# Kernel tuning notes

Measured on AMD Instinct MI355X. Metric: run time of the kernel, lower is better.

The kernel has to match this reference:

```python
import jax, jax.numpy as jnp
import numpy as np

# Sizes: N news nodes, E 'similar' edges, 768-d input, hidden 64, 4 heads, 2 HGT layers, 2 classes
N, E, F_IN, HID, H, L, C = 100000, 1600000, 768, 64, 4, 2, 2
D = HID // H  # per-head dim = 16


def setup_inputs() -> dict:
    key = jax.random.key(0)
    ks = jax.random.split(key, 16)
    s = 0.05
    nrm = lambda k, shape: jax.random.normal(k, shape, jnp.float32) * s
    return {
        "x": jax.random.normal(ks[0], (N, F_IN), jnp.float32),
        "edge_index": jax.random.randint(ks[1], (2, E), 0, N, jnp.int32),
        # input projection
        "Wp": nrm(ks[2], (F_IN, HID)), "bp": jnp.zeros((HID,), jnp.float32),
        # per-layer HGT params (stacked over L layers)
        "Wk": nrm(ks[3], (L, HID, HID)), "bk": jnp.zeros((L, HID), jnp.float32),
        "Wq": nrm(ks[4], (L, HID, HID)), "bq": jnp.zeros((L, HID), jnp.float32),
        "Wv": nrm(ks[5], (L, HID, HID)), "bv": jnp.zeros((L, HID), jnp.float32),
        "a_rel": nrm(ks[6], (L, H, D, D)),  # per-edge-type attention transform
        "m_rel": nrm(ks[7], (L, H, D, D)),  # per-edge-type message transform
        "p_rel": jnp.ones((L, H), jnp.float32),  # relation prior
        "Wo": nrm(ks[8], (L, HID, HID)), "bo": jnp.zeros((L, HID), jnp.float32),
        "skip": jnp.ones((L,), jnp.float32),
        # classifier MLP: 64 -> 32 -> 2
        "Wc1": nrm(ks[9], (HID, HID // 2)), "bc1": jnp.zeros((HID // 2,), jnp.float32),
        "Wc2": nrm(ks[10], (HID // 2, C)), "bc2": jnp.zeros((C,), jnp.float32),
    }


def _hgt_layer(h, src, dst, Wk, bk, Wq, bq, Wv, bv, a_rel, m_rel, p_rel, Wo, bo, skip):
    n = h.shape[0]
    k = (h @ Wk + bk).reshape(n, H, D)
    q = (h @ Wq + bq).reshape(n, H, D)
    v = (h @ Wv + bv).reshape(n, H, D)
    # per-edge attention logits: (k_src @ a_rel) . q_dst * p_rel / sqrt(D)
    k_e = jnp.einsum('ehd,hdf->ehf', k[src], a_rel)          # [E,H,D]
    alpha = jnp.einsum('ehf,ehf->eh', k_e, q[dst]) * p_rel / np.float32(np.sqrt(D))
    # segment softmax over incoming edges of each dst node
    mx = jax.ops.segment_max(alpha, dst, num_segments=n)     # [N,H]
    a = jnp.exp(alpha - mx[dst])
    denom = jax.ops.segment_sum(a, dst, num_segments=n)
    a = a / (denom[dst] + 1e-16)
    # messages + scatter-add aggregation
    msg = jnp.einsum('ehd,hdf->ehf', v[src], m_rel)          # [E,H,D]
    agg = jax.ops.segment_sum(a[..., None] * msg, dst, num_segments=n).reshape(n, HID)
    out = jax.nn.gelu(agg) @ Wo + bo
    g = jax.nn.sigmoid(skip)
    return g * out + (1.0 - g) * h  # skip connection (same dims)


def reference(x, edge_index, Wp, bp, Wk, bk, Wq, bq, Wv, bv, a_rel, m_rel, p_rel,
              Wo, bo, skip, Wc1, bc1, Wc2, bc2):
    src, dst = edge_index[0], edge_index[1]
    h = x @ Wp + bp
    for l in range(L):
        h = _hgt_layer(h, src, dst, Wk[l], bk[l], Wq[l], bq[l], Wv[l], bv[l],
                       a_rel[l], m_rel[l], p_rel[l], Wo[l], bo[l], skip[l])
        h = jax.nn.relu(h)  # dropout is identity in eval mode
    hc = jax.nn.relu(h @ Wc1 + bc1)
    return hc @ Wc2 + bc2  # [N, C] logits
```

## Files before the change

kernel.cpp:

```cpp
#include <hip/hip_runtime.h>
#include <math.h>


typedef __attribute__((ext_vector_type(8))) short bf16x8;
typedef __attribute__((ext_vector_type(4))) float f32x4;

__device__ __forceinline__ float gelu_t(float x) {
  const float c = 0.7978845608028654f;
  float t = tanhf(c * (x + 0.044715f * x * x * x));
  return 0.5f * x * (1.0f + t);
}

__device__ __forceinline__ void split1(float a, ushort& h, ushort& l) {
  unsigned u = __float_as_uint(a);
  unsigned uh = u & 0xffff0000u;
  float fl = a - __uint_as_float(uh);
  h = (ushort)(uh >> 16);
  l = (ushort)(__float_as_uint(fl) >> 16);
}

template<int K, bool PRE_GELU, bool EPI_SKIP>
__global__ __launch_bounds__(256, 4)
void mfma_gemm(const float* __restrict__ A, int ldA,
               const ushort* __restrict__ Wt,
               const float* __restrict__ bias,
               const float* __restrict__ Hprev,
               const float* __restrict__ skipPtr,
               float* __restrict__ outp, int ldOut, int nRows)
{
  constexpr int NCH = K / 32;
  __shared__ ushort sA[2 * 64 * 32];
  __shared__ ushort sB[2 * 64 * 32];
  const int tid = threadIdx.x;
  const int lane = tid & 63;
  const int wv = tid >> 6;
  const int m = lane & 15;
  const int q = lane >> 4;
  const int row0 = blockIdx.x * 64;
  const int colBlk = blockIdx.y * 64;

  const int srow = tid >> 2;
  const int skoff = (tid & 3) * 8;
  int gr = row0 + srow; if (gr >= nRows) gr = nRows - 1;
  const float* aBase = A + (size_t)gr * ldA + skoff;
  const float4* wBase = (const float4*)(Wt + (size_t)blockIdx.y * NCH * 4096);

  f32x4 acc[4];
#pragma unroll
  for (int ct = 0; ct < 4; ++ct) acc[ct] = (f32x4){0.f, 0.f, 0.f, 0.f};

  float4 a0 = *(const float4*)(aBase + 0);
  float4 a1 = *(const float4*)(aBase + 4);
  float4 b0 = wBase[tid * 2];
  float4 b1 = wBase[tid * 2 + 1];

#pragma clang loop unroll(disable)
  for (int ch = 0; ch < NCH; ++ch) {
    float4 na0 = a0, na1 = a1, nb0 = b0, nb1 = b1;
    if (ch + 1 < NCH) {
      na0 = *(const float4*)(aBase + (ch + 1) * 32);
      na1 = *(const float4*)(aBase + (ch + 1) * 32 + 4);
      const float4* wc = wBase + (size_t)(ch + 1) * 512;
      nb0 = wc[tid * 2];
      nb1 = wc[tid * 2 + 1];
    }
    float av[8] = {a0.x, a0.y, a0.z, a0.w, a1.x, a1.y, a1.z, a1.w};
    if (PRE_GELU) {
#pragma unroll
      for (int j = 0; j < 8; ++j) av[j] = gelu_t(av[j]);
    }
    bf16x8 vh, vl;
#pragma unroll
    for (int j = 0; j < 8; ++j) {
      ushort h, l; split1(av[j], h, l);
      vh[j] = (short)h; vl[j] = (short)l;
    }
    __syncthreads();
    *(bf16x8*)(sA + srow * 32 + skoff) = vh;
    *(bf16x8*)(sA + 2048 + srow * 32 + skoff) = vl;
    ((float4*)sB)[tid * 2] = b0;
    ((float4*)sB)[tid * 2 + 1] = b1;
    __syncthreads();
    bf16x8 ah = *(const bf16x8*)(sA + (wv * 16 + m) * 32 + q * 8);
    bf16x8 al = *(const bf16x8*)(sA + 2048 + (wv * 16 + m) * 32 + q * 8);
#pragma unroll
    for (int ct = 0; ct < 4; ++ct) {
      bf16x8 bh = *(const bf16x8*)(sB + (ct * 16 + m) * 32 + q * 8);
      bf16x8 bl = *(const bf16x8*)(sB + 2048 + (ct * 16 + m) * 32 + q * 8);
      acc[ct] = __builtin_amdgcn_mfma_f32_16x16x32_bf16(ah, bh, acc[ct], 0, 0, 0);
      acc[ct] = __builtin_amdgcn_mfma_f32_16x16x32_bf16(ah, bl, acc[ct], 0, 0, 0);
      acc[ct] = __builtin_amdgcn_mfma_f32_16x16x32_bf16(al, bh, acc[ct], 0, 0, 0);
    }
    a0 = na0; a1 = na1; b0 = nb0; b1 = nb1;
  }

  float g = 0.f, gi = 0.f;
  if (EPI_SKIP) { g = 1.0f / (1.0f + __expf(-skipPtr[0])); gi = 1.0f - g; }
#pragma unroll
  for (int ct = 0; ct < 4; ++ct) {
    int c = colBlk + ct * 16 + m;
    float b = bias[c];
#pragma unroll
    for (int i = 0; i < 4; ++i) {
      int r = row0 + wv * 16 + q * 4 + i;
      if (r < nRows) {
        float o = acc[ct][i] + b;
        if (EPI_SKIP) {
          float hp = Hprev[(size_t)r * 64 + c];
          o = fmaxf(g * o + gi * hp, 0.f);
        }
        outp[(size_t)r * ldOut + c] = o;
      }
    }
  }
}

__global__ void prep_weights(const float* __restrict__ W, int K, int C,
                             ushort* __restrict__ Wt)
{
  int idx = blockIdx.x * 256 + threadIdx.x;
  if (idx < K * C) {
    int k = idx / C, c = idx % C;
    ushort h, l; split1(W[idx], h, l);
    int cb = c >> 6, cc = c & 63, ch = k >> 5, kk = k & 31;
    size_t base = (size_t)(cb * (K >> 5) + ch) * 4096;
    Wt[base + cc * 32 + kk] = h;
    Wt[base + 2048 + cc * 32 + kk] = l;
  }
}

__global__ void fold_weights(const float* __restrict__ Wq, const float* __restrict__ bq,
                             const float* __restrict__ Wk, const float* __restrict__ bk,
                             const float* __restrict__ Wv, const float* __restrict__ bv,
                             const float* __restrict__ a_rel, const float* __restrict__ m_rel,
                             float* __restrict__ Wqkv, float* __restrict__ bqkv)
{
  int l = blockIdx.x;
  const float* wq = Wq + l * 4096; const float* wk = Wk + l * 4096; const float* wv = Wv + l * 4096;
  const float* bql = bq + l * 64;  const float* bkl = bk + l * 64;  const float* bvl = bv + l * 64;
  const float* ar = a_rel + l * 1024; const float* mr = m_rel + l * 1024;
  float* W = Wqkv + l * 64 * 192;  float* B = bqkv + l * 192;
  for (int t = threadIdx.x; t < 64 * 192; t += blockDim.x) {
    int i = t / 192, c = t % 192;
    float val;
    int cp;
    if (c < 64) {
      val = wq[i * 64 + c];
      cp = c;
    } else if (c < 128) {
      int cc = c - 64, hh = cc >> 4, f = cc & 15;
      float s = 0.f;
      for (int d = 0; d < 16; ++d) s += wk[i * 64 + hh * 16 + d] * ar[hh * 256 + d * 16 + f];
      val = s;
      cp = 64 + (cc << 1);
    } else {
      int cc = c - 128, hh = cc >> 4, f = cc & 15;
      float s = 0.f;
      for (int d = 0; d < 16; ++d) s += wv[i * 64 + hh * 16 + d] * mr[hh * 256 + d * 16 + f];
      val = s;
      cp = 64 + (cc << 1) + 1;
    }
    W[i * 192 + cp] = val;
  }
  for (int c = threadIdx.x; c < 192; c += blockDim.x) {
    float val;
    int cp;
    if (c < 64) {
      val = bql[c];
      cp = c;
    } else if (c < 128) {
      int cc = c - 64, hh = cc >> 4, f = cc & 15;
      float s = 0.f;
      for (int d = 0; d < 16; ++d) s += bkl[hh * 16 + d] * ar[hh * 256 + d * 16 + f];
      val = s;
      cp = 64 + (cc << 1);
    } else {
      int cc = c - 128, hh = cc >> 4, f = cc & 15;
      float s = 0.f;
      for (int d = 0; d < 16; ++d) s += bvl[hh * 16 + d] * mr[hh * 256 + d * 16 + f];
      val = s;
      cp = 64 + (cc << 1) + 1;
    }
    B[cp] = val;
  }
}

__global__ void hist_kernel(const int* __restrict__ dst, int* __restrict__ counts, int E) {
  int e = blockIdx.x * 256 + threadIdx.x;
  if (e < E) atomicAdd(&counts[dst[e]], 1);
}

__global__ __launch_bounds__(256)
void scanA(int* __restrict__ counts, int* __restrict__ blockSums, int n) {
  __shared__ int sd[256];
  int tid = threadIdx.x;
  int base = blockIdx.x * 1024 + tid * 4;
  int v[4];
#pragma unroll
  for (int j = 0; j < 4; ++j) v[j] = (base + j < n) ? counts[base + j] : 0;
  int t = v[0] + v[1] + v[2] + v[3];
  sd[tid] = t; __syncthreads();
  for (int offm = 1; offm < 256; offm <<= 1) {
    int adj = (tid >= offm) ? sd[tid - offm] : 0;
    __syncthreads();
    sd[tid] += adj;
    __syncthreads();
  }
  int run = sd[tid] - t;
#pragma unroll
  for (int j = 0; j < 4; ++j) {
    if (base + j < n) counts[base + j] = run;
    run += v[j];
  }
  if (tid == 255) blockSums[blockIdx.x] = sd[255];
}

__global__ void scanB(int* __restrict__ blockSums, int G, int* __restrict__ row_ptr, int n) {
  __shared__ int sd[128];
  int tid = threadIdx.x;
  int t = (tid < G) ? blockSums[tid] : 0;
  sd[tid] = t; __syncthreads();
  for (int offm = 1; offm < 128; offm <<= 1) {
    int adj = (tid >= offm) ? sd[tid - offm] : 0;
    __syncthreads();
    sd[tid] += adj;
    __syncthreads();
  }
  if (tid < G) blockSums[tid] = sd[tid] - t;
  if (tid == 127) row_ptr[n] = sd[127];
}

__global__ void scanC(const int* __restrict__ counts, const int* __restrict__ blockSums,
                      int* __restrict__ row_ptr, int* __restrict__ cursor, int n) {
  int idx = blockIdx.x * 256 + threadIdx.x;
  if (idx < n) {
    int v = counts[idx] + blockSums[idx >> 10];
    row_ptr[idx] = v;
    cursor[idx] = v;
  }
}

__global__ void scatter_kernel(const int* __restrict__ src, const int* __restrict__ dst,
                               int* __restrict__ cursor, int* __restrict__ csr_src, int E) {
  int e = blockIdx.x * 256 + threadIdx.x;
  if (e < E) {
    int d = dst[e];
    int pos = atomicAdd(&cursor[d], 1);
    csr_src[pos] = src[e];
  }
}

__global__ __launch_bounds__(256)
void edge_agg(const float* __restrict__ qkv, const int* __restrict__ row_ptr,
              const int* __restrict__ csr_src, const float* __restrict__ p_rel,
              float* __restrict__ agg, int n)
{
  int wid = blockIdx.x * 4 + (threadIdx.x >> 6);
  if (wid >= n) return;
  int lane = threadIdx.x & 63;
  int head = lane >> 4;
  float pr = p_rel[head] * 0.25f;
  float qv = qkv[(size_t)wid * 192 + lane] * pr;
  int e0 = row_ptr[wid], e1 = row_ptr[wid + 1];
  float num = 0.f, den = 0.f;
  for (int e = e0; e < e1; e += 4) {
    int last = e1 - 1;
    int ia = e;
    int ib = (e + 1 < e1) ? e + 1 : last;
    int ic = (e + 2 < e1) ? e + 2 : last;
    int id = (e + 3 < e1) ? e + 3 : last;
    int s0 = csr_src[ia];
    int s1 = csr_src[ib];
    int s2 = csr_src[ic];
    int s3 = csr_src[id];
    float2 kv0 = *(const float2*)(qkv + (size_t)s0 * 192 + 64 + 2 * lane);
    float2 kv1 = *(const float2*)(qkv + (size_t)s1 * 192 + 64 + 2 * lane);
    float2 kv2 = *(const float2*)(qkv + (size_t)s2 * 192 + 64 + 2 * lane);
    float2 kv3 = *(const float2*)(qkv + (size_t)s3 * 192 + 64 + 2 * lane);
    float p0 = kv0.x * qv;
    float p1 = kv1.x * qv;
    float p2 = kv2.x * qv;
    float p3 = kv3.x * qv;
#pragma unroll
    for (int o = 1; o < 16; o <<= 1) {
      p0 += __shfl_xor(p0, o);
      p1 += __shfl_xor(p1, o);
      p2 += __shfl_xor(p2, o);
      p3 += __shfl_xor(p3, o);
    }
    float w0 = __expf(p0);
    float w1 = (e + 1 < e1) ? __expf(p1) : 0.f;
    float w2 = (e + 2 < e1) ? __expf(p2) : 0.f;
    float w3 = (e + 3 < e1) ? __expf(p3) : 0.f;
    den += (w0 + w1) + (w2 + w3);
    num = fmaf(w0, kv0.y, num);
    num = fmaf(w1, kv1.y, num);
    num = fmaf(w2, kv2.y, num);
    num = fmaf(w3, kv3.y, num);
  }
  agg[(size_t)wid * 64 + lane] = num / (den + 1e-16f);
}

__global__ __launch_bounds__(256)
void classifier(const float* __restrict__ h, const float* __restrict__ Wc1,
                const float* __restrict__ bc1, const float* __restrict__ Wc2,
                const float* __restrict__ bc2, float* __restrict__ out, int n)
{
  int row = blockIdx.x * 256 + threadIdx.x;
  if (row >= n) return;
  float hid[32];
#pragma unroll
  for (int j = 0; j < 32; ++j) hid[j] = bc1[j];
  const float* hr = h + (size_t)row * 64;
#pragma unroll 4
  for (int k = 0; k < 64; k += 4) {
    float4 x = *(const float4*)&hr[k];
#pragma unroll
    for (int j = 0; j < 32; ++j) {
      hid[j] += x.x * Wc1[k * 32 + j] + x.y * Wc1[(k + 1) * 32 + j]
              + x.z * Wc1[(k + 2) * 32 + j] + x.w * Wc1[(k + 3) * 32 + j];
    }
  }
  float o0 = bc2[0], o1 = bc2[1];
#pragma unroll
  for (int j = 0; j < 32; ++j) {
    float v = fmaxf(hid[j], 0.f);
    o0 += v * Wc2[j * 2 + 0];
    o1 += v * Wc2[j * 2 + 1];
  }
  *(float2*)&out[(size_t)row * 2] = make_float2(o0, o1);
}

extern "C" void kernel_launch(void* const* d_in, const int* in_sizes, int n_in,
                              void* d_out, int out_size, void* d_ws, size_t ws_size,
                              hipStream_t stream)
{
  const float* x     = (const float*)d_in[0];
  const int*  eidx   = (const int*)d_in[1];
  const float* Wp    = (const float*)d_in[2];
  const float* bp    = (const float*)d_in[3];
  const float* Wk    = (const float*)d_in[4];
  const float* bk    = (const float*)d_in[5];
  const float* Wq    = (const float*)d_in[6];
  const float* bq    = (const float*)d_in[7];
  const float* Wv    = (const float*)d_in[8];
  const float* bv    = (const float*)d_in[9];
  const float* a_rel = (const float*)d_in[10];
  const float* m_rel = (const float*)d_in[11];
  const float* p_rel = (const float*)d_in[12];
  const float* Wo    = (const float*)d_in[13];
  const float* bo    = (const float*)d_in[14];
  const float* skip  = (const float*)d_in[15];
  const float* Wc1   = (const float*)d_in[16];
  const float* bc1   = (const float*)d_in[17];
  const float* Wc2   = (const float*)d_in[18];
  const float* bc2   = (const float*)d_in[19];
  float* out = (float*)d_out;

  const int N = in_sizes[0] / 768;
  const int E = in_sizes[1] / 2;
  const int* srcIdx = eidx;
  const int* dstIdx = eidx + E;

  char* ws = (char*)d_ws;
  size_t off = 0;
  auto alloc = [&](size_t bytes) -> void* {
    void* p = ws + off;
    off = (off + bytes + 255) & ~(size_t)255;
    return p;
  };
  float* h     = (float*)alloc((size_t)N * 64 * 4);
  float* qkv   = (float*)alloc((size_t)N * 192 * 4);
  float* agg   = (float*)alloc((size_t)N * 64 * 4);
  float* Wqkv  = (float*)alloc(2 * 64 * 192 * 4);
  float* bqkv  = (float*)alloc(2 * 192 * 4);
  int* row_ptr = (int*)alloc((size_t)(N + 1) * 4);
  int* cursor  = (int*)alloc((size_t)N * 4);
  int* counts  = (int*)alloc((size_t)N * 4);
  int* blockSums = (int*)alloc(512 * 4);
  int* csr_src = (int*)alloc((size_t)E * 4);
  ushort* WtP   = (ushort*)alloc((size_t)64 * 768 * 2 * 2);
  ushort* WtQKV = (ushort*)alloc((size_t)2 * 192 * 64 * 2 * 2);
  ushort* WtO   = (ushort*)alloc((size_t)2 * 64 * 64 * 2 * 2);
  (void)ws_size; (void)n_in; (void)out_size;

  hipMemsetAsync(counts, 0, (size_t)N * 4, stream);

  fold_weights<<<2, 256, 0, stream>>>(Wq, bq, Wk, bk, Wv, bv, a_rel, m_rel, Wqkv, bqkv);

  prep_weights<<<(768 * 64 + 255) / 256, 256, 0, stream>>>(Wp, 768, 64, WtP);
  for (int l = 0; l < 2; ++l) {
    prep_weights<<<(64 * 192 + 255) / 256, 256, 0, stream>>>(
        Wqkv + l * 64 * 192, 64, 192, WtQKV + (size_t)l * 192 * 64 * 2);
    prep_weights<<<(64 * 64 + 255) / 256, 256, 0, stream>>>(
        Wo + l * 4096, 64, 64, WtO + (size_t)l * 64 * 64 * 2);
  }

  mfma_gemm<768, false, false><<<dim3((N + 63) / 64, 1), 256, 0, stream>>>(
      x, 768, WtP, bp, nullptr, nullptr, h, 64, N);

  hist_kernel<<<(E + 255) / 256, 256, 0, stream>>>(dstIdx, counts, E);
  int G = (N + 1023) / 1024;
  scanA<<<G, 256, 0, stream>>>(counts, blockSums, N);
  scanB<<<1, 128, 0, stream>>>(blockSums, G, row_ptr, N);
  scanC<<<(N + 255) / 256, 256, 0, stream>>>(counts, blockSums, row_ptr, cursor, N);
  scatter_kernel<<<(E + 255) / 256, 256, 0, stream>>>(srcIdx, dstIdx, cursor, csr_src, E);

  for (int l = 0; l < 2; ++l) {
    mfma_gemm<64, false, false><<<dim3((N + 63) / 64, 3), 256, 0, stream>>>(
        h, 64, WtQKV + (size_t)l * 192 * 64 * 2, bqkv + l * 192,
        nullptr, nullptr, qkv, 192, N);
    edge_agg<<<(N + 3) / 4, 256, 0, stream>>>(qkv, row_ptr, csr_src, p_rel + l * 4, agg, N);
    mfma_gemm<64, true, true><<<dim3((N + 63) / 64, 1), 256, 0, stream>>>(
        agg, 64, WtO + (size_t)l * 64 * 64 * 2, bo + l * 64, h, skip + l, h, 64, N);
  }

  classifier<<<(N + 255) / 256, 256, 0, stream>>>(h, Wc1, bc1, Wc2, bc2, out, N);
}
```

Baseline: 1.054 ms.

## Add specialized K=64 MFMA GEMM and unroll edge aggregation with DPP reductions

Adds a K=64-specialized split-bf16 MFMA GEMM. It loads the whole A tile once and computes all 192 QKV columns in one block instead of three grid columns, which avoids re-reading and re-splitting A per column block. The edge aggregation kernel now processes 8 edges per iteration and uses readfirstlane to make the neighbor indices scalar. Its 16-lane dot-product reduction uses DPP row_ror instead of shuffles. This raises register and LDS use (launch bounds drop to 2) in exchange for fewer redundant loads and more memory-level parallelism.

After: 1.071 ms. About the same (+1.6%).

```diff
diff --git a/kernel.cpp b/kernel.cpp
--- a/kernel.cpp
+++ b/kernel.cpp
@@ -17,6 +17,19 @@
   float fl = a - __uint_as_float(uh);
   h = (ushort)(uh >> 16);
   l = (ushort)(__float_as_uint(fl) >> 16);
+}
+
+template<int CTRL>
+__device__ __forceinline__ float row_ror_add(float v) {
+  int r = __builtin_amdgcn_update_dpp(0, __float_as_int(v), CTRL, 0xF, 0xF, true);
+  return v + __int_as_float(r);
+}
+__device__ __forceinline__ float red16(float v) {
+  v = row_ror_add<0x121>(v);
+  v = row_ror_add<0x122>(v);
+  v = row_ror_add<0x124>(v);
+  v = row_ror_add<0x128>(v);
+  return v;
 }
 
 template<int K, bool PRE_GELU, bool EPI_SKIP>
@@ -110,6 +123,125 @@
           o = fmaxf(g * o + gi * hp, 0.f);
         }
         outp[(size_t)r * ldOut + c] = o;
+      }
+    }
+  }
+}
+
+template<int CB, bool PRE_GELU, bool EPI_SKIP>
+__global__ __launch_bounds__(256, 2)
+void mfma_gemm_k64(const float* __restrict__ A,
+                   const ushort* __restrict__ Wt,
+                   const float* __restrict__ bias,
+                   const float* __restrict__ Hprev,
+                   const float* __restrict__ skipPtr,
+                   float* __restrict__ outp, int ldOut, int nRows)
+{
+  __shared__ ushort sA[2 * 4096];
+  __shared__ ushort sB[CB][2 * 4096];
+  const int tid = threadIdx.x;
+  const int lane = tid & 63;
+  const int wv = tid >> 6;
+  const int m = lane & 15;
+  const int q = lane >> 4;
+  const int row0 = blockIdx.x * 64;
+  const int srow = tid >> 2;
+  const int skoff = (tid & 3) * 8;
+  int gr = row0 + srow; if (gr >= nRows) gr = nRows - 1;
+  const float* aBase = A + (size_t)gr * 64 + skoff;
+  const float4* wBase = (const float4*)Wt;
+
+  float4 a0 = *(const float4*)(aBase + 0);
+  float4 a1 = *(const float4*)(aBase + 4);
+  float4 a2 = *(const float4*)(aBase + 32);
+  float4 a3 = *(const float4*)(aBase + 36);
+  float4 bb0[CB], bb1[CB], bb2[CB], bb3[CB];
+#pragma unroll
+  for (int cb = 0; cb < CB; ++cb) {
+    bb0[cb] = wBase[(size_t)(cb * 2 + 0) * 512 + tid * 2];
+    bb1[cb] = wBase[(size_t)(cb * 2 + 0) * 512 + tid * 2 + 1];
+    bb2[cb] = wBase[(size_t)(cb * 2 + 1) * 512 + tid * 2];
+    bb3[cb] = wBase[(size_t)(cb * 2 + 1) * 512 + tid * 2 + 1];
+  }
+
+  {
+    float av[16] = {a0.x, a0.y, a0.z, a0.w, a1.x, a1.y, a1.z, a1.w,
+                    a2.x, a2.y, a2.z, a2.w, a3.x, a3.y, a3.z, a3.w};
+    if (PRE_GELU) {
+#pragma unroll
+      for (int j = 0; j < 16; ++j) av[j] = gelu_t(av[j]);
+    }
+    bf16x8 vh0, vl0, vh1, vl1;
+#pragma unroll
+    for (int j = 0; j < 8; ++j) {
+      ushort h, l; split1(av[j], h, l);
+      vh0[j] = (short)h; vl0[j] = (short)l;
+    }
+#pragma unroll
+    for (int j = 0; j < 8; ++j) {
+      ushort h, l; split1(av[8 + j], h, l);
+      vh1[j] = (short)h; vl1[j] = (short)l;
+    }
+    *(bf16x8*)(sA + srow * 32 + skoff) = vh0;
+    *(bf16x8*)(sA + 2048 + srow * 32 + skoff) = vl0;
+    *(bf16x8*)(sA + 4096 + srow * 32 + skoff) = vh1;
+    *(bf16x8*)(sA + 4096 + 2048 + srow * 32 + skoff) = vl1;
+  }
+#pragma unroll
+  for (int cb = 0; cb < CB; ++cb) {
+    ((float4*)(sB[cb]))[tid * 2] = bb0[cb];
+    ((float4*)(sB[cb]))[tid * 2 + 1] = bb1[cb];
+    ((float4*)(sB[cb] + 4096))[tid * 2] = bb2[cb];
+    ((float4*)(sB[cb] + 4096))[tid * 2 + 1] = bb3[cb];
+  }
+  __syncthreads();
+
+  f32x4 acc[CB][4];
+#pragma unroll
+  for (int cb = 0; cb < CB; ++cb)
+#pragma unroll
+    for (int ct = 0; ct < 4; ++ct) acc[cb][ct] = (f32x4){0.f, 0.f, 0.f, 0.f};
+
+  bf16x8 ah0 = *(const bf16x8*)(sA + (wv * 16 + m) * 32 + q * 8);
+  bf16x8 al0 = *(const bf16x8*)(sA + 2048 + (wv * 16 + m) * 32 + q * 8);
+  bf16x8 ah1 = *(const bf16x8*)(sA + 4096 + (wv * 16 + m) * 32 + q * 8);
+  bf16x8 al1 = *(const bf16x8*)(sA + 4096 + 2048 + (wv * 16 + m) * 32 + q * 8);
+#pragma unroll
+  for (int cb = 0; cb < CB; ++cb) {
+#pragma unroll
+    for (int ct = 0; ct < 4; ++ct) {
+      bf16x8 bh0 = *(const bf16x8*)(sB[cb] + (ct * 16 + m) * 32 + q * 8);
+      bf16x8 bl0 = *(const bf16x8*)(sB[cb] + 2048 + (ct * 16 + m) * 32 + q * 8);
+      acc[cb][ct] = __builtin_amdgcn_mfma_f32_16x16x32_bf16(ah0, bh0, acc[cb][ct], 0, 0, 0);
+      acc[cb][ct] = __builtin_amdgcn_mfma_f32_16x16x32_bf16(ah0, bl0, acc[cb][ct], 0, 0, 0);
+      acc[cb][ct] = __builtin_amdgcn_mfma_f32_16x16x32_bf16(al0, bh0, acc[cb][ct], 0, 0, 0);
+      bf16x8 bh1 = *(const bf16x8*)(sB[cb] + 4096 + (ct * 16 + m) * 32 + q * 8);
+      bf16x8 bl1 = *(const bf16x8*)(sB[cb] + 4096 + 2048 + (ct * 16 + m) * 32 + q * 8);
+      acc[cb][ct] = __builtin_amdgcn_mfma_f32_16x16x32_bf16(ah1, bh1, acc[cb][ct], 0, 0, 0);
+      acc[cb][ct] = __builtin_amdgcn_mfma_f32_16x16x32_bf16(ah1, bl1, acc[cb][ct], 0, 0, 0);
+      acc[cb][ct] = __builtin_amdgcn_mfma_f32_16x16x32_bf16(al1, bh1, acc[cb][ct], 0, 0, 0);
+    }
+  }
+
+  float g = 0.f, gi = 0.f;
+  if (EPI_SKIP) { g = 1.0f / (1.0f + __expf(-skipPtr[0])); gi = 1.0f - g; }
+#pragma unroll
+  for (int cb = 0; cb < CB; ++cb) {
+#pragma unroll
+    for (int ct = 0; ct < 4; ++ct) {
+      int c = cb * 64 + ct * 16 + m;
+      float b = bias[c];
+#pragma unroll
+      for (int i = 0; i < 4; ++i) {
+        int r = row0 + wv * 16 + q * 4 + i;
+        if (r < nRows) {
+          float o = acc[cb][ct][i] + b;
+          if (EPI_SKIP) {
+            float hp = Hprev[(size_t)r * 64 + c];
+            o = fmaxf(g * o + gi * hp, 0.f);
+          }
+          outp[(size_t)r * ldOut + c] = o;
+        }
       }
     }
   }
@@ -261,42 +393,60 @@
   int head = lane >> 4;
   float pr = p_rel[head] * 0.25f;
   float qv = qkv[(size_t)wid * 192 + lane] * pr;
-  int e0 = row_ptr[wid], e1 = row_ptr[wid + 1];
+  int e0 = __builtin_amdgcn_readfirstlane(row_ptr[wid]);
+  int e1 = __builtin_amdgcn_readfirstlane(row_ptr[wid + 1]);
+  const float* ktb = qkv + 64 + 2 * lane;
   float num = 0.f, den = 0.f;
-  for (int e = e0; e < e1; e += 4) {
+  for (int e = e0; e < e1; e += 8) {
     int last = e1 - 1;
-    int ia = e;
-    int ib = (e + 1 < e1) ? e + 1 : last;
-    int ic = (e + 2 < e1) ? e + 2 : last;
-    int id = (e + 3 < e1) ? e + 3 : last;
-    int s0 = csr_src[ia];
-    int s1 = csr_src[ib];
-    int s2 = csr_src[ic];
-    int s3 = csr_src[id];
-    float2 kv0 = *(const float2*)(qkv + (size_t)s0 * 192 + 64 + 2 * lane);
-    float2 kv1 = *(const float2*)(qkv + (size_t)s1 * 192 + 64 + 2 * lane);
-    float2 kv2 = *(const float2*)(qkv + (size_t)s2 * 192 + 64 + 2 * lane);
-    float2 kv3 = *(const float2*)(qkv + (size_t)s3 * 192 + 64 + 2 * lane);
-    float p0 = kv0.x * qv;
-    float p1 = kv1.x * qv;
-    float p2 = kv2.x * qv;
-    float p3 = kv3.x * qv;
-#pragma unroll
-    for (int o = 1; o < 16; o <<= 1) {
-      p0 += __shfl_xor(p0, o);
-      p1 += __shfl_xor(p1, o);
-      p2 += __shfl_xor(p2, o);
-      p3 += __shfl_xor(p3, o);
-    }
+    int i1 = (e + 1 < e1) ? e + 1 : last;
+    int i2 = (e + 2 < e1) ? e + 2 : last;
+    int i3 = (e + 3 < e1) ? e + 3 : last;
+    int i4 = (e + 4 < e1) ? e + 4 : last;
+    int i5 = (e + 5 < e1) ? e + 5 : last;
+    int i6 = (e + 6 < e1) ? e + 6 : last;
+    int i7 = (e + 7 < e1) ? e + 7 : last;
+    int s0 = __builtin_amdgcn_readfirstlane(csr_src[e]);
+    int s1 = __builtin_amdgcn_readfirstlane(csr_src[i1]);
+    int s2 = __builtin_amdgcn_readfirstlane(csr_src[i2]);
+    int s3 = __builtin_amdgcn_readfirstlane(csr_src[i3]);
+    int s4 = __builtin_amdgcn_readfirstlane(csr_src[i4]);
+    int s5 = __builtin_amdgcn_readfirstlane(csr_src[i5]);
+    int s6 = __builtin_amdgcn_readfirstlane(csr_src[i6]);
+    int s7 = __builtin_amdgcn_readfirstlane(csr_src[i7]);
+    float2 kv0 = *(const float2*)(ktb + (size_t)s0 * 192);
+    float2 kv1 = *(const float2*)(ktb + (size_t)s1 * 192);
+    float2 kv2 = *(const float2*)(ktb + (size_t)s2 * 192);
+    float2 kv3 = *(const float2*)(ktb + (size_t)s3 * 192);
+    float2 kv4 = *(const float2*)(ktb + (size_t)s4 * 192);
+    float2 kv5 = *(const float2*)(ktb + (size_t)s5 * 192);
+    float2 kv6 = *(const float2*)(ktb + (size_t)s6 * 192);
+    float2 kv7 = *(const float2*)(ktb + (size_t)s7 * 192);
+    float p0 = red16(kv0.x * qv);
+    float p1 = red16(kv1.x * qv);
+    float p2 = red16(kv2.x * qv);
+    float p3 = red16(kv3.x * qv);
+    float p4 = red16(kv4.x * qv);
+    float p5 = red16(kv5.x * qv);
+    float p6 = red16(kv6.x * qv);
+    float p7 = red16(kv7.x * qv);
     float w0 = __expf(p0);
     float w1 = (e + 1 < e1) ? __expf(p1) : 0.f;
     float w2 = (e + 2 < e1) ? __expf(p2) : 0.f;
     float w3 = (e + 3 < e1) ? __expf(p3) : 0.f;
-    den += (w0 + w1) + (w2 + w3);
+    float w4 = (e + 4 < e1) ? __expf(p4) : 0.f;
+    float w5 = (e + 5 < e1) ? __expf(p5) : 0.f;
+    float w6 = (e + 6 < e1) ? __expf(p6) : 0.f;
+    float w7 = (e + 7 < e1) ? __expf(p7) : 0.f;
+    den += ((w0 + w1) + (w2 + w3)) + ((w4 + w5) + (w6 + w7));
     num = fmaf(w0, kv0.y, num);
     num = fmaf(w1, kv1.y, num);
     num = fmaf(w2, kv2.y, num);
     num = fmaf(w3, kv3.y, num);
+    num = fmaf(w4, kv4.y, num);
+    num = fmaf(w5, kv5.y, num);
+    num = fmaf(w6, kv6.y, num);
+    num = fmaf(w7, kv7.y, num);
   }
   agg[(size_t)wid * 64 + lane] = num / (den + 1e-16f);
 }
@@ -407,12 +557,12 @@
   scatter_kernel<<<(E + 255) / 256, 256, 0, stream>>>(srcIdx, dstIdx, cursor, csr_src, E);
 
   for (int l = 0; l < 2; ++l) {
-    mfma_gemm<64, false, false><<<dim3((N + 63) / 64, 3), 256, 0, stream>>>(
-        h, 64, WtQKV + (size_t)l * 192 * 64 * 2, bqkv + l * 192,
+    mfma_gemm_k64<3, false, false><<<(N + 63) / 64, 256, 0, stream>>>(
+        h, WtQKV + (size_t)l * 192 * 64 * 2, bqkv + l * 192,
         nullptr, nullptr, qkv, 192, N);
     edge_agg<<<(N + 3) / 4, 256, 0, stream>>>(qkv, row_ptr, csr_src, p_rel + l * 4, agg, N);
-    mfma_gemm<64, true, true><<<dim3((N + 63) / 64, 1), 256, 0, stream>>>(
-        agg, 64, WtO + (size_t)l * 64 * 64 * 2, bo + l * 64, h, skip + l, h, 64, N);
+    mfma_gemm_k64<1, true, true><<<(N + 63) / 64, 256, 0, stream>>>(
+        agg, WtO + (size_t)l * 64 * 64 * 2, bo + l * 64, h, skip + l, h, 64, N);
   }
 
   classifier<<<(N + 255) / 256, 256, 0, stream>>>(h, Wc1, bc1, Wc2, bc2, out, N);
```
